# Optimization experiments

Measured on AMD Instinct MI355X. Metric: run time of the kernel, lower is better.

The kernel has to match this reference:

```python
import jax, jax.numpy as jnp
import numpy as np

MINIMUM_VALUE = -1e9  # C.MINIMUM_VALUE: large negative fill for masked positions


def setup_inputs() -> dict:
    key = jax.random.key(0)
    kq, kv, km, kw = jax.random.split(key, 4)
    B, N, H = 8, 2048, 1024
    query = jax.random.normal(kq, (B, N, H), dtype=jnp.float32)
    value = jax.random.normal(kv, (B, N, H), dtype=jnp.float32)
    mask = jax.random.randint(km, (B, N, N), 0, 2, dtype=jnp.int32)
    W = jax.random.normal(kw, (H, H), dtype=jnp.float32)
    return {"query": query, "value": value, "mask": mask, "W": W}


def reference(query, value, mask, W):
    # intermediate = query @ W           : B x M x H
    # e = relu(intermediate @ value^T)   : B x M x N
    e = jax.nn.relu(jnp.einsum("bmh,hk,bnk->bmn", query, W, value))
    attn_logits = jnp.where(mask > 0, e, MINIMUM_VALUE)
    attn = jax.nn.softmax(attn_logits, axis=-1)
    output = jnp.einsum("bmn,bnh->bmh", attn, value)
    return (output, attn)
```

## Files before the change

### kernel.cpp

```cpp
#include <hip/hip_runtime.h>


typedef _Float16 half8 __attribute__((ext_vector_type(8)));
typedef float f32x4 __attribute__((ext_vector_type(4)));
typedef unsigned short u16;
typedef unsigned int u32;

#define BATCH 8
#define SEQ   2048
#define HID   1024
#define MINV  (-1e9f)

#define AS1 __attribute__((address_space(1)))
#define AS3 __attribute__((address_space(3)))

__device__ __forceinline__ u16 h2u(_Float16 h) { return __builtin_bit_cast(u16, h); }

__device__ __forceinline__ u32 packhl(float x) {
    _Float16 h = (_Float16)x;
    _Float16 l = (_Float16)(x - (float)h);
    return (u32)h2u(h) | ((u32)h2u(l) << 16);
}

__device__ __forceinline__ void gload16(const char* g, AS3 char* l) {
    __builtin_amdgcn_global_load_lds((const AS1 void*)g, (AS3 void*)l, 16, 0, 0);
}

__global__ __launch_bounds__(256) void prep_v(const float* __restrict__ V,
                                              u16* __restrict__ Vp,
                                              u16* __restrict__ Vt)
{
    __shared__ __align__(16) u16 lt[64 * 72];
    const int b = blockIdx.z, n0 = blockIdx.y * 64, h0 = blockIdx.x * 64;
    const int t = threadIdx.x;
    const int r = t >> 4, c4 = (t & 15) * 4;
#pragma unroll
    for (int it = 0; it < 4; ++it) {
        const int rr = r + it * 16;
        const float4 x = *(const float4*)(V + ((size_t)b * SEQ + n0 + rr) * HID + h0 + c4);
        const float xs[4] = {x.x, x.y, x.z, x.w};
        u32 p[4];
#pragma unroll
        for (int e = 0; e < 4; ++e) {
            p[e] = packhl(xs[e]);
            lt[(c4 + e) * 72 + rr] = (u16)p[e];
        }
        const int g = (h0 + c4) >> 5, j = c4 & 31;
        u16* base = Vp + (((size_t)b * SEQ + n0 + rr) * 32 + g) * 64;
        *(uint2*)(base + j) = make_uint2((p[0] & 0xffffu) | (p[1] << 16),
                                         (p[2] & 0xffffu) | (p[3] << 16));
        *(uint2*)(base + 32 + j) = make_uint2((p[0] >> 16) | (p[1] & 0xffff0000u),
                                              (p[2] >> 16) | (p[3] & 0xffff0000u));
    }
    __syncthreads();
    const int hr = t >> 2, cc = (t & 3) * 2;
    uint4 v0 = *(const uint4*)&lt[hr * 72 + cc * 8];
    uint4 v1 = *(const uint4*)&lt[hr * 72 + cc * 8 + 8];
    u16* dst = Vt + ((size_t)b * HID + h0 + hr) * SEQ + n0 + cc * 8;
    *(uint4*)dst = v0;
    *(uint4*)(dst + 8) = v1;
}

__global__ __launch_bounds__(256) void prep_w(const float* __restrict__ W,
                                              u16* __restrict__ Wtp)
{
    __shared__ __align__(16) u32 lt[64 * 68];
    const int n0 = blockIdx.x * 64, k0 = blockIdx.y * 64;
    const int t = threadIdx.x;
    const int r = t >> 4, c4 = (t & 15) * 4;
#pragma unroll
    for (int it = 0; it < 4; ++it) {
        const int rr = r + it * 16;
        const float4 x = *(const float4*)(W + (size_t)(k0 + rr) * HID + n0 + c4);
        const float xs[4] = {x.x, x.y, x.z, x.w};
#pragma unroll
        for (int e = 0; e < 4; ++e) lt[(c4 + e) * 68 + rr] = packhl(xs[e]);
    }
    __syncthreads();
    const int n = t >> 2;
#pragma unroll
    for (int s = 0; s < 4; ++s) {
        const int ci = (t & 3) + s * 4;
        uint4 v = *(const uint4*)&lt[n * 68 + ci * 4];
        const int k = k0 + ci * 4;
        u16* base = Wtp + (((size_t)n0 + n) * 32 + (k >> 5)) * 64;
        const int j = k & 31;
        *(uint2*)(base + j) = make_uint2((v.x & 0xffffu) | (v.y << 16),
                                         (v.z & 0xffffu) | (v.w << 16));
        *(uint2*)(base + 32 + j) = make_uint2((v.x >> 16) | (v.y & 0xffff0000u),
                                              (v.z >> 16) | (v.w & 0xffff0000u));
    }
}

__global__ __launch_bounds__(256) void prep_q(const float* __restrict__ Q,
                                              u16* __restrict__ Qp)
{
    const size_t row = blockIdx.x;
    const int t = threadIdx.x;
    const float4 x = ((const float4*)(Q + row * HID))[t];
    const u32 p0 = packhl(x.x), p1 = packhl(x.y), p2 = packhl(x.z), p3 = packhl(x.w);
    const int k = t * 4;
    u16* base = Qp + (row * 32 + (k >> 5)) * 64;
    const int j = k & 31;
    *(uint2*)(base + j) = make_uint2((p0 & 0xffffu) | (p1 << 16),
                                     (p2 & 0xffffu) | (p3 << 16));
    *(uint2*)(base + 32 + j) = make_uint2((p0 >> 16) | (p1 & 0xffff0000u),
                                          (p2 >> 16) | (p3 & 0xffff0000u));
}

template <bool SPLIT>
__device__ __forceinline__ void mfma_block(f32x4 (&acc)[8][4], int p,
                                           const half8 (&ah)[2], const half8 (&al)[2],
                                           const half8 (&bh)[4], const half8 (&bl)[4])
{
#pragma unroll
    for (int j = 0; j < 4; ++j)
#pragma unroll
        for (int e = 0; e < 2; ++e) {
            f32x4 c = acc[p * 2 + e][j];
            if constexpr (SPLIT) {
                c = __builtin_amdgcn_mfma_f32_16x16x32_f16(al[e], bh[j], c, 0, 0, 0);
                c = __builtin_amdgcn_mfma_f32_16x16x32_f16(ah[e], bl[j], c, 0, 0, 0);
                c = __builtin_amdgcn_mfma_f32_16x16x32_f16(ah[e], bh[j], c, 0, 0, 0);
            } else {
                c = __builtin_amdgcn_mfma_f32_16x16x32_f16(ah[e], bh[j], c, 0, 0, 0);
                c = __builtin_amdgcn_mfma_f32_16x16x32_f16(al[e], bl[j], c, 0, 0, 0);
            }
            acc[p * 2 + e][j] = c;
        }
}

template <int MODE>
__global__ __launch_bounds__(512, 2) void gemm_mfma(
    const char* __restrict__ Abase, const char* __restrict__ Bbase,
    void* __restrict__ Cbase, const int* __restrict__ Mbase,
    int ldc, long sAb, long sBb, long sC, long sM)
{
    constexpr bool SPLIT = (MODE != 3);
    extern __shared__ __align__(16) char smem[];

    const int nx = gridDim.x, ny = gridDim.y;
    const int nxy = nx * ny;
    int wg = blockIdx.x + nx * (blockIdx.y + ny * blockIdx.z);
    const int cpx = (nxy * gridDim.z) >> 3;
    wg = (wg & 7) * cpx + (wg >> 3);
    const int bz = wg / nxy;
    const int rem = wg - bz * nxy;
    const int m0 = (rem / nx) * 256, n0 = (rem % nx) * 256;

    const int tid = threadIdx.x;
    const int w = tid >> 6, l = tid & 63;
    const int wm = w >> 2, wn = w & 3;
    const int lm = l & 15, q = l >> 4;

    const char* Ab = Abase + (long)bz * sAb;
    const char* Bb = Bbase + (long)bz * sBb;

    size_t aoffs[4], boffs[4];
    int dsto[4];
#pragma unroll
    for (int it = 0; it < 4; ++it) {
        const int off = it * 8192 + tid * 16;
        dsto[it] = off;
        const int row = off >> 7;
        const int swi = (off & 127) ^ ((row & 7) << 4);
        aoffs[it] = (size_t)(m0 + row) * 4096 + swi;
        boffs[it] = (size_t)(n0 + row) * 4096 + swi;
    }
    const int wofs = (q * 16) ^ ((lm & 7) << 4);

    f32x4 acc[8][4];
#pragma unroll
    for (int i = 0; i < 8; ++i)
#pragma unroll
        for (int j = 0; j < 4; ++j) acc[i][j] = (f32x4){0.f, 0.f, 0.f, 0.f};

    AS3 char* lds = (AS3 char*)smem;

#pragma unroll
    for (int it = 0; it < 4; ++it) gload16(Ab + aoffs[it], lds + dsto[it]);
#pragma unroll
    for (int it = 0; it < 4; ++it) gload16(Bb + boffs[it], lds + 32768 + dsto[it]);
    asm volatile("s_waitcnt vmcnt(0)" ::: "memory");
    __builtin_amdgcn_s_barrier();

    half8 bh[4], bl[4], ah[2], al[2];

    for (int ks = 0; ks < 32; ++ks) {
        const int cur = ks & 1;
        const char* At = smem + cur * 65536;
        const char* Bt = At + 32768;

#pragma unroll
        for (int j = 0; j < 4; ++j) {
            const char* cp = Bt + (wn * 64 + j * 16 + lm) * 128;
            bh[j] = *(const half8*)(cp + wofs);
            bl[j] = *(const half8*)(cp + (wofs ^ 64));
        }
#pragma unroll
        for (int e = 0; e < 2; ++e) {
            const char* rp = At + (wm * 128 + e * 16 + lm) * 128;
            ah[e] = *(const half8*)(rp + wofs);
            al[e] = *(const half8*)(rp + (wofs ^ 64));
        }
        if (ks + 1 < 32) {
            AS3 char* ldsn = lds + (cur ^ 1) * 65536;
            const size_t kb = (size_t)(ks + 1) * 128;
#pragma unroll
            for (int it = 0; it < 4; ++it) gload16(Ab + aoffs[it] + kb, ldsn + dsto[it]);
#pragma unroll
            for (int it = 0; it < 4; ++it) gload16(Bb + boffs[it] + kb, ldsn + 32768 + dsto[it]);
        }
        __builtin_amdgcn_s_barrier();
        asm volatile("s_waitcnt lgkmcnt(0)" ::: "memory");
        __builtin_amdgcn_s_setprio(1);
        mfma_block<SPLIT>(acc, 0, ah, al, bh, bl);
        __builtin_amdgcn_s_setprio(0);
        __builtin_amdgcn_s_barrier();

#pragma unroll
        for (int p = 1; p < 4; ++p) {
#pragma unroll
            for (int e = 0; e < 2; ++e) {
                const char* rp = At + (wm * 128 + (p * 2 + e) * 16 + lm) * 128;
                ah[e] = *(const half8*)(rp + wofs);
                al[e] = *(const half8*)(rp + (wofs ^ 64));
            }
            __builtin_amdgcn_s_barrier();
            asm volatile("s_waitcnt lgkmcnt(0)" ::: "memory");
            __builtin_amdgcn_s_setprio(1);
            mfma_block<SPLIT>(acc, p, ah, al, bh, bl);
            __builtin_amdgcn_s_setprio(0);
            if (p < 3) __builtin_amdgcn_s_barrier();
        }
        asm volatile("s_waitcnt vmcnt(0)" ::: "memory");
        __builtin_amdgcn_s_barrier();
    }

#pragma unroll
    for (int i = 0; i < 8; ++i) {
#pragma unroll
        for (int r = 0; r < 4; ++r) {
            const int grow = m0 + wm * 128 + i * 16 + q * 4 + r;
#pragma unroll
            for (int j = 0; j < 4; ++j) {
                const int gcol = n0 + wn * 64 + j * 16 + lm;
                const float v = acc[i][j][r];
                if constexpr (MODE == 1) {
                    const u32 p = packhl(v);
                    u16* base = (u16*)Cbase + ((size_t)grow * (ldc >> 5) + (gcol >> 5)) * 64;
                    base[gcol & 31] = (u16)p;
                    base[32 + (gcol & 31)] = (u16)(p >> 16);
                } else if constexpr (MODE == 2) {
                    const int mv = Mbase[(long)bz * sM + (long)grow * ldc + gcol];
                    ((float*)Cbase)[(long)bz * sC + (long)grow * ldc + gcol] =
                        (mv > 0) ? fmaxf(v, 0.f) : MINV;
                } else {
                    ((float*)Cbase)[(long)bz * sC + (long)grow * ldc + gcol] = v;
                }
            }
        }
    }
}

__global__ __launch_bounds__(256) void softmax2048(float* __restrict__ attn,
                                                   u16* __restrict__ attnH)
{
    const long row = blockIdx.x;
    float* p = attn + row * 2048;
    const int tid = threadIdx.x;

    float4 v0 = ((const float4*)p)[tid];
    float4 v1 = ((const float4*)p)[tid + 256];

    float mx = fmaxf(fmaxf(fmaxf(v0.x, v0.y), fmaxf(v0.z, v0.w)),
                     fmaxf(fmaxf(v1.x, v1.y), fmaxf(v1.z, v1.w)));
#pragma unroll
    for (int o = 32; o >= 1; o >>= 1)
        mx = fmaxf(mx, __shfl_xor(mx, o, 64));

    __shared__ float redm[4];
    __shared__ float reds[4];
    const int wid = tid >> 6, lane = tid & 63;
    if (lane == 0) redm[wid] = mx;
    __syncthreads();
    mx = fmaxf(fmaxf(redm[0], redm[1]), fmaxf(redm[2], redm[3]));

    float e[8];
    e[0] = __expf(v0.x - mx); e[1] = __expf(v0.y - mx);
    e[2] = __expf(v0.z - mx); e[3] = __expf(v0.w - mx);
    e[4] = __expf(v1.x - mx); e[5] = __expf(v1.y - mx);
    e[6] = __expf(v1.z - mx); e[7] = __expf(v1.w - mx);

    float s = ((e[0] + e[1]) + (e[2] + e[3])) + ((e[4] + e[5]) + (e[6] + e[7]));
#pragma unroll
    for (int o = 32; o >= 1; o >>= 1)
        s += __shfl_xor(s, o, 64);
    if (lane == 0) reds[wid] = s;
    __syncthreads();
    s = (reds[0] + reds[1]) + (reds[2] + reds[3]);

    const float inv = 1.0f / s;
    float o0 = e[0] * inv, o1 = e[1] * inv, o2 = e[2] * inv, o3 = e[3] * inv;
    float o4 = e[4] * inv, o5 = e[5] * inv, o6 = e[6] * inv, o7 = e[7] * inv;
    ((float4*)p)[tid]       = make_float4(o0, o1, o2, o3);
    ((float4*)p)[tid + 256] = make_float4(o4, o5, o6, o7);

    u16* ph = attnH + row * 2048;
    ((uint2*)ph)[tid] =
        make_uint2((u32)h2u((_Float16)o0) | ((u32)h2u((_Float16)o1) << 16),
                   (u32)h2u((_Float16)o2) | ((u32)h2u((_Float16)o3) << 16));
    ((uint2*)ph)[tid + 256] =
        make_uint2((u32)h2u((_Float16)o4) | ((u32)h2u((_Float16)o5) << 16),
                   (u32)h2u((_Float16)o6) | ((u32)h2u((_Float16)o7) << 16));
}

extern "C" void kernel_launch(void* const* d_in, const int* in_sizes, int n_in,
                              void* d_out, int out_size, void* d_ws, size_t ws_size,
                              hipStream_t stream)
{
    (void)in_sizes; (void)n_in; (void)out_size; (void)ws_size;

    const float* query = (const float*)d_in[0];
    const float* value = (const float*)d_in[1];
    const int*   mask  = (const int*)d_in[2];
    const float* W     = (const float*)d_in[3];

    float* out  = (float*)d_out;
    float* attn = out + (size_t)BATCH * SEQ * HID;

    u16* Vp  = (u16*)d_ws;
    u16* Vt  = (u16*)((char*)d_ws + ((size_t)64 << 20));
    u16* Wtp = (u16*)((char*)d_ws + ((size_t)96 << 20));

    u16* interP = (u16*)d_out;
    u16* Qp     = (u16*)attn;
    u16* attnH  = Vp;

    static int attr_done = 0;
    if (!attr_done) {
        hipFuncSetAttribute((const void*)gemm_mfma<1>,
                            hipFuncAttributeMaxDynamicSharedMemorySize, 131072);
        hipFuncSetAttribute((const void*)gemm_mfma<2>,
                            hipFuncAttributeMaxDynamicSharedMemorySize, 131072);
        hipFuncSetAttribute((const void*)gemm_mfma<3>,
                            hipFuncAttributeMaxDynamicSharedMemorySize, 131072);
        attr_done = 1;
    }

    prep_v<<<dim3(HID / 64, SEQ / 64, BATCH), 256, 0, stream>>>(value, Vp, Vt);
    prep_w<<<dim3(HID / 64, HID / 64, 1), 256, 0, stream>>>(W, Wtp);
    prep_q<<<dim3(BATCH * SEQ), 256, 0, stream>>>(query, Qp);

    gemm_mfma<1><<<dim3(HID / 256, (BATCH * SEQ) / 256, 1), 512, 131072, stream>>>(
        (const char*)Qp, (const char*)Wtp, interP, nullptr,
        HID, 0, 0, 0, 0);

    gemm_mfma<2><<<dim3(SEQ / 256, SEQ / 256, BATCH), 512, 131072, stream>>>(
        (const char*)interP, (const char*)Vp, attn, mask,
        SEQ, (long)SEQ * 4096, (long)SEQ * 4096, (long)SEQ * SEQ, (long)SEQ * SEQ);

    softmax2048<<<dim3(BATCH * SEQ), 256, 0, stream>>>(attn, attnH);

    gemm_mfma<3><<<dim3(HID / 256, SEQ / 256, BATCH), 512, 131072, stream>>>(
        (const char*)attnH, (const char*)Vt, out, nullptr,
        HID, (long)SEQ * 4096, (long)HID * 4096, (long)SEQ * HID, 0);
}
```

Measured before the change: 738.3 us.

## Restructure GEMM main loop into four interleaved quadrant clusters with split prefetch

The main MFMA loop is rebuilt around four 4x2 fragment clusters, with each wave's tile positions remapped into interleaved quadrants. Fewer A/B fragments are held in registers at once (4 A plus 4 B pairs). The global-to-LDS prefetch of the next K slice is split into pieces placed between clusters, with partial vmcnt waits and sched_barriers. The aim is to overlap global loads and LDS reads with MFMA work more evenly and to cut register pressure. The cost is a more fragile wait/barrier schedule and a changed output index mapping.

```diff
diff --git a/kernel.cpp b/kernel.cpp
--- a/kernel.cpp
+++ b/kernel.cpp
@@ -109,25 +109,28 @@
 }
 
 template <bool SPLIT>
-__device__ __forceinline__ void mfma_block(f32x4 (&acc)[8][4], int p,
-                                           const half8 (&ah)[2], const half8 (&al)[2],
-                                           const half8 (&bh)[4], const half8 (&bl)[4])
-{
-#pragma unroll
-    for (int j = 0; j < 4; ++j)
-#pragma unroll
-        for (int e = 0; e < 2; ++e) {
-            f32x4 c = acc[p * 2 + e][j];
+__device__ __forceinline__ void cluster4x2(f32x4 (&acc)[8][4], int ib, int jb,
+                                           const half8 (&ah)[4], const half8 (&al)[4],
+                                           half8 bh0, half8 bl0, half8 bh1, half8 bl1)
+{
+#pragma unroll
+    for (int f = 0; f < 4; ++f) {
+#pragma unroll
+        for (int jj = 0; jj < 2; ++jj) {
+            const half8 bh = jj ? bh1 : bh0;
+            const half8 bl = jj ? bl1 : bl0;
+            f32x4 c = acc[ib + f][jb + jj];
             if constexpr (SPLIT) {
-                c = __builtin_amdgcn_mfma_f32_16x16x32_f16(al[e], bh[j], c, 0, 0, 0);
-                c = __builtin_amdgcn_mfma_f32_16x16x32_f16(ah[e], bl[j], c, 0, 0, 0);
-                c = __builtin_amdgcn_mfma_f32_16x16x32_f16(ah[e], bh[j], c, 0, 0, 0);
+                c = __builtin_amdgcn_mfma_f32_16x16x32_f16(al[f], bh, c, 0, 0, 0);
+                c = __builtin_amdgcn_mfma_f32_16x16x32_f16(ah[f], bl, c, 0, 0, 0);
+                c = __builtin_amdgcn_mfma_f32_16x16x32_f16(ah[f], bh, c, 0, 0, 0);
             } else {
-                c = __builtin_amdgcn_mfma_f32_16x16x32_f16(ah[e], bh[j], c, 0, 0, 0);
-                c = __builtin_amdgcn_mfma_f32_16x16x32_f16(al[e], bl[j], c, 0, 0, 0);
+                c = __builtin_amdgcn_mfma_f32_16x16x32_f16(ah[f], bh, c, 0, 0, 0);
+                c = __builtin_amdgcn_mfma_f32_16x16x32_f16(al[f], bl, c, 0, 0, 0);
             }
-            acc[p * 2 + e][j] = c;
-        }
+            acc[ib + f][jb + jj] = c;
+        }
+    }
 }
 
 template <int MODE>
@@ -184,67 +187,107 @@
     asm volatile("s_waitcnt vmcnt(0)" ::: "memory");
     __builtin_amdgcn_s_barrier();
 
-    half8 bh[4], bl[4], ah[2], al[2];
+    half8 ah[4], al[4];
+    half8 b0h, b0l, b1h, b1l, b2h, b2l, b3h, b3l;
 
     for (int ks = 0; ks < 32; ++ks) {
         const int cur = ks & 1;
         const char* At = smem + cur * 65536;
         const char* Bt = At + 32768;
-
-#pragma unroll
-        for (int j = 0; j < 4; ++j) {
-            const char* cp = Bt + (wn * 64 + j * 16 + lm) * 128;
-            bh[j] = *(const half8*)(cp + wofs);
-            bl[j] = *(const half8*)(cp + (wofs ^ 64));
-        }
-#pragma unroll
-        for (int e = 0; e < 2; ++e) {
-            const char* rp = At + (wm * 128 + e * 16 + lm) * 128;
-            ah[e] = *(const half8*)(rp + wofs);
-            al[e] = *(const half8*)(rp + (wofs ^ 64));
-        }
-        if (ks + 1 < 32) {
-            AS3 char* ldsn = lds + (cur ^ 1) * 65536;
-            const size_t kb = (size_t)(ks + 1) * 128;
-#pragma unroll
-            for (int it = 0; it < 4; ++it) gload16(Ab + aoffs[it] + kb, ldsn + dsto[it]);
-#pragma unroll
-            for (int it = 0; it < 4; ++it) gload16(Bb + boffs[it] + kb, ldsn + 32768 + dsto[it]);
+        AS3 char* ldsA = lds + (cur ^ 1) * 65536;
+        AS3 char* ldsB = ldsA + 32768;
+        const size_t kb = (size_t)(ks + 1) * 128;
+        const bool more = (ks < 31);
+
+#pragma unroll
+        for (int i = 0; i < 4; ++i) {
+            const char* rp = At + ((i >> 1) * 64 + wm * 32 + (i & 1) * 16 + lm) * 128;
+            ah[i] = *(const half8*)(rp + wofs);
+            al[i] = *(const half8*)(rp + (wofs ^ 64));
+        }
+        {
+            const char* cp0 = Bt + (wn * 32 + lm) * 128;
+            b0h = *(const half8*)(cp0 + wofs);
+            b0l = *(const half8*)(cp0 + (wofs ^ 64));
+            const char* cp1 = Bt + (wn * 32 + 16 + lm) * 128;
+            b1h = *(const half8*)(cp1 + wofs);
+            b1l = *(const half8*)(cp1 + (wofs ^ 64));
+        }
+        if (more) {
+            gload16(Ab + aoffs[0] + kb, ldsA + dsto[0]);
+            gload16(Ab + aoffs[1] + kb, ldsA + dsto[1]);
+            gload16(Bb + boffs[0] + kb, ldsB + dsto[0]);
+            gload16(Bb + boffs[1] + kb, ldsB + dsto[1]);
+            asm volatile("s_waitcnt vmcnt(6)" ::: "memory");
+        } else {
+            asm volatile("s_waitcnt vmcnt(2)" ::: "memory");
         }
         __builtin_amdgcn_s_barrier();
         asm volatile("s_waitcnt lgkmcnt(0)" ::: "memory");
+        __builtin_amdgcn_sched_barrier(0);
         __builtin_amdgcn_s_setprio(1);
-        mfma_block<SPLIT>(acc, 0, ah, al, bh, bl);
+        cluster4x2<SPLIT>(acc, 0, 0, ah, al, b0h, b0l, b1h, b1l);
         __builtin_amdgcn_s_setprio(0);
         __builtin_amdgcn_s_barrier();
 
-#pragma unroll
-        for (int p = 1; p < 4; ++p) {
-#pragma unroll
-            for (int e = 0; e < 2; ++e) {
-                const char* rp = At + (wm * 128 + (p * 2 + e) * 16 + lm) * 128;
-                ah[e] = *(const half8*)(rp + wofs);
-                al[e] = *(const half8*)(rp + (wofs ^ 64));
-            }
-            __builtin_amdgcn_s_barrier();
-            asm volatile("s_waitcnt lgkmcnt(0)" ::: "memory");
-            __builtin_amdgcn_s_setprio(1);
-            mfma_block<SPLIT>(acc, p, ah, al, bh, bl);
-            __builtin_amdgcn_s_setprio(0);
-            if (p < 3) __builtin_amdgcn_s_barrier();
-        }
-        asm volatile("s_waitcnt vmcnt(0)" ::: "memory");
+        {
+            const char* cp2 = Bt + (128 + wn * 32 + lm) * 128;
+            b2h = *(const half8*)(cp2 + wofs);
+            b2l = *(const half8*)(cp2 + (wofs ^ 64));
+            const char* cp3 = Bt + (128 + wn * 32 + 16 + lm) * 128;
+            b3h = *(const half8*)(cp3 + wofs);
+            b3l = *(const half8*)(cp3 + (wofs ^ 64));
+        }
+        if (more) {
+            gload16(Bb + boffs[2] + kb, ldsB + dsto[2]);
+            gload16(Bb + boffs[3] + kb, ldsB + dsto[3]);
+            asm volatile("s_waitcnt vmcnt(6)" ::: "memory");
+        } else {
+            asm volatile("s_waitcnt vmcnt(0)" ::: "memory");
+        }
+        __builtin_amdgcn_s_barrier();
+        asm volatile("s_waitcnt lgkmcnt(0)" ::: "memory");
+        __builtin_amdgcn_sched_barrier(0);
+        __builtin_amdgcn_s_setprio(1);
+        cluster4x2<SPLIT>(acc, 0, 2, ah, al, b2h, b2l, b3h, b3l);
+        __builtin_amdgcn_s_setprio(0);
+        __builtin_amdgcn_s_barrier();
+
+#pragma unroll
+        for (int i = 0; i < 4; ++i) {
+            const char* rp = At + (128 + (i >> 1) * 64 + wm * 32 + (i & 1) * 16 + lm) * 128;
+            ah[i] = *(const half8*)(rp + wofs);
+            al[i] = *(const half8*)(rp + (wofs ^ 64));
+        }
+        if (more) {
+            gload16(Ab + aoffs[2] + kb, ldsA + dsto[2]);
+            gload16(Ab + aoffs[3] + kb, ldsA + dsto[3]);
+        }
+        __builtin_amdgcn_s_barrier();
+        asm volatile("s_waitcnt lgkmcnt(0)" ::: "memory");
+        __builtin_amdgcn_sched_barrier(0);
+        __builtin_amdgcn_s_setprio(1);
+        cluster4x2<SPLIT>(acc, 4, 2, ah, al, b2h, b2l, b3h, b3l);
+        __builtin_amdgcn_s_setprio(0);
+        __builtin_amdgcn_s_barrier();
+
+        if (more) asm volatile("s_waitcnt vmcnt(4)" ::: "memory");
+        __builtin_amdgcn_s_barrier();
+        __builtin_amdgcn_s_setprio(1);
+        cluster4x2<SPLIT>(acc, 4, 0, ah, al, b0h, b0l, b1h, b1l);
+        __builtin_amdgcn_s_setprio(0);
         __builtin_amdgcn_s_barrier();
     }
 
 #pragma unroll
     for (int i = 0; i < 8; ++i) {
+        const int arow = (i >> 1) * 64 + wm * 32 + (i & 1) * 16 + q * 4;
 #pragma unroll
         for (int r = 0; r < 4; ++r) {
-            const int grow = m0 + wm * 128 + i * 16 + q * 4 + r;
+            const int grow = m0 + arow + r;
 #pragma unroll
             for (int j = 0; j < 4; ++j) {
-                const int gcol = n0 + wn * 64 + j * 16 + lm;
+                const int gcol = n0 + (j >> 1) * 128 + wn * 32 + (j & 1) * 16 + lm;
                 const float v = acc[i][j][r];
                 if constexpr (MODE == 1) {
                     const u32 p = packhl(v);
```

After: 717.2 us. 1.03x faster.
